# Kernel optimization log

Measured on AMD Instinct MI355X. Metric: run time of the kernel, lower is better.

The kernel has to match this reference:

```python
import jax, jax.numpy as jnp
import numpy as np

DIM = 96
D_STATE = 16
EXPAND = 2
D_INNER = EXPAND * DIM
DT_RANK = (DIM + 15) // 16  # 6
B, H, W = 2, 64, 64
K = 4  # scan directions


def _ln(x, w, b, eps=1e-5):
    mu = x.mean(-1, keepdims=True)
    var = x.var(-1, keepdims=True)
    return (x - mu) / jnp.sqrt(var + eps) * w + b


def setup_inputs() -> dict:
    key = jax.random.key(0)
    ks = jax.random.split(key, 10)
    f = jnp.float32
    x = jax.random.normal(ks[0], (B, H, W, DIM), dtype=f)
    y = jax.random.normal(ks[1], (B, H, W, DIM), dtype=f)
    inp = {
        'x': x,
        'y': y,
        'ln_w': jnp.ones((DIM,), f),
        'ln_b': jnp.zeros((DIM,), f),
        'in_proj_w': jax.random.normal(ks[2], (2 * D_INNER, DIM), f) * 0.05,
        'conv_w': jax.random.normal(ks[3], (D_INNER, 1, 3, 3), f) * 0.1,
        'conv_b': jnp.zeros((D_INNER,), f),
        'x_proj_w': jax.random.normal(ks[4], (K, DT_RANK + 2 * D_STATE, D_INNER), f) * 0.05,
        'dt_w': jax.random.normal(ks[5], (K, D_INNER, DT_RANK), f) * 0.1,
        'dt_b': jax.random.normal(ks[6], (K, D_INNER), f) * 0.1,
        'A_log': jnp.broadcast_to(jnp.log(jnp.arange(1, D_STATE + 1, dtype=f)), (K, D_INNER, D_STATE)),
        'Ds': jnp.ones((K, D_INNER), f),
        'out_norm_w': jnp.ones((D_INNER,), f),
        'out_norm_b': jnp.zeros((D_INNER,), f),
        'out_proj_w': jax.random.normal(ks[7], (DIM, D_INNER), f) * 0.05,
    }
    return inp


def _fwd(x, y, ln_w, ln_b, in_proj_w, conv_w, conv_b, x_proj_w, dt_w, dt_b,
         A_log, Ds, out_norm_w, out_norm_b, out_proj_w):
    Bsz, Hh, Ww, C = x.shape
    Din = conv_w.shape[0]
    N = A_log.shape[-1]
    R = dt_w.shape[-1]
    L = Hh * Ww

    diff = jnp.abs(x - y)                       # TemporalSpectrumBlock abs-diff
    h = _ln(diff, ln_w, ln_b)                   # VSSBlock ln_1
    xz = h @ in_proj_w.T                        # (B,H,W,2*Din)
    xm, z = jnp.split(xz, 2, axis=-1)
    xm = xm.transpose(0, 3, 1, 2)               # (B,Din,H,W)
    xm = jax.lax.conv_general_dilated(
        xm, conv_w, (1, 1), 'SAME', feature_group_count=Din,
        dimension_numbers=('NCHW', 'OIHW', 'NCHW')) + conv_b[None, :, None, None]
    xm = jax.nn.silu(xm)

    # 4-directional sequences (B,4,Din,L)
    x0 = xm.reshape(Bsz, Din, L)
    x1 = xm.transpose(0, 1, 3, 2).reshape(Bsz, Din, L)
    xs = jnp.stack([x0, x1], axis=1)
    xs = jnp.concatenate([xs, jnp.flip(xs, axis=-1)], axis=1)

    x_dbl = jnp.einsum('bkdl,kcd->bkcl', xs, x_proj_w)
    dts, Bs, Cs = jnp.split(x_dbl, [R, R + N], axis=2)   # (B,4,R,L),(B,4,N,L),(B,4,N,L)
    dts = jnp.einsum('bkrl,kdr->bkdl', dts, dt_w)
    delta = jax.nn.softplus(dts + dt_b[None, :, :, None])  # (B,4,Din,L)

    A = -jnp.exp(A_log)                                    # (4,Din,N)
    dA = jnp.exp(delta[..., None] * A[None, :, :, None, :])          # (B,4,Din,L,N)
    dBu = delta[..., None] * Bs.transpose(0, 1, 3, 2)[:, :, None] * xs[..., None]

    dA_t = dA.transpose(3, 0, 1, 2, 4)    # (L,B,4,Din,N)
    dBu_t = dBu.transpose(3, 0, 1, 2, 4)
    C_t = Cs.transpose(3, 0, 1, 2)        # (L,B,4,N)
    h0 = jnp.zeros((Bsz, 4, Din, N), dtype=x.dtype)

    def step(hc, inp):
        a, bu, c = inp
        hc = a * hc + bu
        yv = jnp.einsum('bkdn,bkn->bkd', hc, c)
        return hc, yv

    _, ys = jax.lax.scan(step, h0, (dA_t, dBu_t, C_t))    # (L,B,4,Din)
    ys = ys.transpose(1, 2, 3, 0)                          # (B,4,Din,L)
    out_y = ys + Ds[None, :, :, None] * xs

    inv_y = jnp.flip(out_y[:, 2:4], axis=-1)
    wh_y = out_y[:, 1].reshape(Bsz, Din, Ww, Hh).transpose(0, 1, 3, 2).reshape(Bsz, Din, L)
    invwh_y = inv_y[:, 1].reshape(Bsz, Din, Ww, Hh).transpose(0, 1, 3, 2).reshape(Bsz, Din, L)
    yc = out_y[:, 0] + inv_y[:, 0] + wh_y + invwh_y        # (B,Din,L)
    yc = yc.transpose(0, 2, 1).reshape(Bsz, Hh, Ww, Din)

    yn = _ln(yc, out_norm_w, out_norm_b)
    out = (yn * jax.nn.silu(z)) @ out_proj_w.T
    return diff + out                                      # residual around the block


def reference(x, y, ln_w, ln_b, in_proj_w, conv_w, conv_b, x_proj_w, dt_w, dt_b,
              A_log, Ds, out_norm_w, out_norm_b, out_proj_w):
    return _fwd(x, y, ln_w, ln_b, in_proj_w, conv_w, conv_b, x_proj_w, dt_w, dt_b,
                A_log, Ds, out_norm_w, out_norm_b, out_proj_w)
```

## Files before the change

### kernel.cpp

```cpp
#include <hip/hip_runtime.h>
#include <math.h>

#define DIMC 96
#define DIN  192
#define NST  16
#define RNK  6
#define KD   4
#define HH   64
#define WWD  64
#define LL   4096
#define BB   2
#define NC   128
#define CH   32
#define CPK  48

__device__ __forceinline__ int pos_of(int k, int l) {
    int t = ((l & 63) << 6) | (l >> 6);
    switch (k) {
        case 0: return l;
        case 1: return t;
        case 2: return LL - 1 - l;
        default: return ((((LL-1-l) & 63) << 6) | ((LL-1-l) >> 6));
    }
}

__device__ __forceinline__ float silu_f(float v) {
    return v / (1.f + __expf(-v));
}

__global__ __launch_bounds__(256) void k0_prep(
    const float* __restrict__ Win, const float* __restrict__ Wout,
    const float* __restrict__ xpw,
    float* __restrict__ WinT, float* __restrict__ WoutT, float* __restrict__ wT3)
{
    int idx = blockIdx.x*256 + threadIdx.x;
    int stride = gridDim.x*256;
    for (int i = idx; i < 96*384; i += stride) {
        int j = i / 384, o = i - j*384;
        WinT[i] = Win[o*96 + j];
    }
    for (int i = idx; i < 192*96; i += stride) {
        int j = i / 96, o = i - j*96;
        WoutT[i] = Wout[o*192 + j];
    }
    for (int i = idx; i < KD*192*CPK; i += stride) {
        int kk = i / (192*CPK); int rem = i - kk*192*CPK;
        int j = rem / CPK, c = rem - j*CPK;
        float v = 0.f;
        if (c < 16)       v = xpw[((size_t)kk*(RNK+2*NST) + RNK + c)*DIN + j];
        else if (c < 32)  v = xpw[((size_t)kk*(RNK+2*NST) + RNK + NST + (c-16))*DIN + j];
        else if (c < 38)  v = xpw[((size_t)kk*(RNK+2*NST) + (c-32))*DIN + j];
        wT3[i] = v;
    }
}

__global__ __launch_bounds__(1024) void k1_ln_inproj(
    const float* __restrict__ x, const float* __restrict__ y,
    const float* __restrict__ lnw, const float* __restrict__ lnb,
    const float* __restrict__ WinT,
    float* __restrict__ diff, float* __restrict__ xm, float* __restrict__ zbuf)
{
    __shared__ float hT[96*65];
    __shared__ float ps1[16*64], ps2[16*64];
    __shared__ float mus[64], rss[64];
    int t = threadIdx.x;
    int ptile = blockIdx.x >> 1, cgrp = blockIdx.x & 1;
    int p0 = ptile*64;

    #pragma unroll
    for (int s = 0; s < 6; s++) {
        int i = t + 1024*s;
        float v = fabsf(x[(size_t)p0*96 + i] - y[(size_t)p0*96 + i]);
        if (cgrp == 0) diff[(size_t)p0*96 + i] = v;
        int pos = i / 96, ch = i - pos*96;
        hT[ch*65 + pos] = v;
    }
    __syncthreads();
    {
        int pos = t & 63, part = t >> 6;
        float s1 = 0.f, s2 = 0.f;
        #pragma unroll
        for (int m = 0; m < 6; m++) {
            float v = hT[(part*6 + m)*65 + pos];
            s1 += v; s2 += v*v;
        }
        ps1[part*64 + pos] = s1; ps2[part*64 + pos] = s2;
    }
    __syncthreads();
    if (t < 64) {
        float S1 = 0.f, S2 = 0.f;
        #pragma unroll
        for (int i = 0; i < 16; i++) { S1 += ps1[i*64 + t]; S2 += ps2[i*64 + t]; }
        float mu = S1 * (1.f/96.f);
        float var = S2 * (1.f/96.f) - mu*mu;
        mus[t] = mu; rss[t] = rsqrtf(var + 1e-5f);
    }
    __syncthreads();
    #pragma unroll
    for (int s = 0; s < 6; s++) {
        int i = t + 1024*s;
        int pos = i / 96, ch = i - pos*96;
        hT[ch*65 + pos] = (hT[ch*65 + pos] - mus[pos]) * rss[pos] * lnw[ch] + lnb[ch];
    }
    __syncthreads();

    int w = __builtin_amdgcn_readfirstlane(t >> 6);
    int lane = t & 63;
    int c0 = cgrp*192 + w*12;
    const float* wp = WinT + c0;
    float acc[12];
    #pragma unroll
    for (int cc = 0; cc < 12; cc++) acc[cc] = 0.f;
    #pragma unroll 2
    for (int j = 0; j < 96; j++) {
        float u = hT[j*65 + lane];
        const float* wrow = wp + j*384;
        #pragma unroll
        for (int cc = 0; cc < 12; cc++) acc[cc] += u * wrow[cc];
    }
    size_t p = (size_t)(p0 + lane);
    float* dst = (c0 < 192) ? (xm + p*192 + c0) : (zbuf + p*192 + (c0 - 192));
    #pragma unroll
    for (int q = 0; q < 3; q++)
        *(float4*)&dst[4*q] = make_float4(acc[4*q], acc[4*q+1], acc[4*q+2], acc[4*q+3]);
}

__global__ __launch_bounds__(192) void k2_conv(
    const float* __restrict__ xm, const float* __restrict__ cw,
    const float* __restrict__ cb, float* __restrict__ xconv)
{
    int p = blockIdx.x;
    int d = threadIdx.x;
    int b = p >> 12;
    int l = p & (LL - 1);
    int hh = l >> 6, ww = l & 63;
    float acc = cb[d];
    const float* wd = cw + d*9;
    #pragma unroll
    for (int di = -1; di <= 1; di++) {
        int h2 = hh + di;
        if ((unsigned)h2 < HH) {
            #pragma unroll
            for (int dj = -1; dj <= 1; dj++) {
                int w2 = ww + dj;
                if ((unsigned)w2 < WWD)
                    acc += wd[(di+1)*3 + (dj+1)] * xm[((size_t)b*LL + h2*WWD + w2)*DIN + d];
            }
        }
    }
    xconv[(size_t)p*DIN + d] = silu_f(acc);
}

__global__ __launch_bounds__(512) void k3_xproj(
    const float* __restrict__ xconv, const float* __restrict__ wT3,
    float* __restrict__ XDK)
{
    __shared__ float uT[192*65];
    int t = threadIdx.x;
    int ptile = blockIdx.x >> 1, wgrp = blockIdx.x & 1;
    int p0 = ptile*64;

    #pragma unroll
    for (int s = 0; s < 24; s++) {
        int i = t + 512*s;
        int pos = i / 192, ch = i - pos*192;
        uT[ch*65 + pos] = xconv[(size_t)(p0 + pos)*192 + ch];
    }
    __syncthreads();

    int w = __builtin_amdgcn_readfirstlane(t >> 6);
    int slot = wgrp*8 + w;
    int k = slot >> 2, cq = slot & 3;
    int lane = t & 63;
    int c0 = cq*12;
    const float* wp = wT3 + (size_t)k*192*CPK + c0;
    float acc[12];
    #pragma unroll
    for (int cc = 0; cc < 12; cc++) acc[cc] = 0.f;
    #pragma unroll 2
    for (int j = 0; j < 192; j++) {
        float u = uT[j*65 + lane];
        const float* wrow = wp + j*CPK;
        #pragma unroll
        for (int cc = 0; cc < 12; cc++) acc[cc] += u * wrow[cc];
    }
    int p = p0 + lane;
    int b = p >> 12;
    int s = p & (LL - 1);
    int ts = ((s & 63) << 6) | (s >> 6);
    int l;
    switch (k) {
        case 0: l = s; break;
        case 1: l = ts; break;
        case 2: l = LL - 1 - s; break;
        default: l = LL - 1 - ts; break;
    }
    float* dst = XDK + ((size_t)(b*KD + k)*LL + l)*CPK + c0;
    #pragma unroll
    for (int q = 0; q < 3; q++)
        *(float4*)&dst[4*q] = make_float4(acc[4*q], acc[4*q+1], acc[4*q+2], acc[4*q+3]);
}

__global__ __launch_bounds__(192) void k4_scanA(
    const float* __restrict__ xconv, const float* __restrict__ XDK,
    const float* __restrict__ dtw, const float* __restrict__ dtb,
    const float* __restrict__ A_log,
    float* __restrict__ Sarr, float* __restrict__ Q)
{
    int blk = blockIdx.x;
    int c  = blk & (NC - 1);
    int bk = blk >> 7;
    int k  = bk & 3;
    int b  = bk >> 2;
    int d  = threadIdx.x;
    float dw[RNK];
    #pragma unroll
    for (int r = 0; r < RNK; r++) dw[r] = dtw[((size_t)k*DIN + d)*RNK + r];
    float bias = dtb[k*DIN + d];
    float A[NST];
    #pragma unroll
    for (int n = 0; n < NST; n++) A[n] = -__expf(A_log[((size_t)k*DIN + d)*NST + n]);
    bool fastA = true;
    #pragma unroll
    for (int n = 1; n < NST; n++)
        fastA = fastA && (fabsf(A[n] - (float)(n+1)*A[0]) <= 1e-4f*(float)(n+1));

    float h[NST];
    #pragma unroll
    for (int n = 0; n < NST; n++) h[n] = 0.f;
    float S = 0.f;

    size_t rb = ((size_t)bk*LL + c*CH)*CPK;
    if (fastA) {
        #pragma unroll 2
        for (int step = 0; step < CH; step++) {
            const float* rec = XDK + rb + step*CPK;
            float dl = bias;
            #pragma unroll
            for (int r = 0; r < RNK; r++) dl += rec[32 + r] * dw[r];
            dl = (dl > 20.f) ? dl : __logf(1.f + __expf(dl));
            int l = c*CH + step;
            float uu = xconv[((size_t)b*LL + pos_of(k, l))*DIN + d];
            float du = dl * uu;
            S += dl;
            float e1 = __expf(dl * A[0]);
            float e2 = e1*e1, e4 = e2*e2;
            float p0 = e1, p1 = e2, p2 = e2*e1, p3 = e4;
            #pragma unroll
            for (int g = 0; g < 4; g++) {
                h[4*g+0] = p0*h[4*g+0] + du*rec[4*g+0];
                h[4*g+1] = p1*h[4*g+1] + du*rec[4*g+1];
                h[4*g+2] = p2*h[4*g+2] + du*rec[4*g+2];
                h[4*g+3] = p3*h[4*g+3] + du*rec[4*g+3];
                if (g < 3) { p0 *= e4; p1 *= e4; p2 *= e4; p3 *= e4; }
            }
        }
    } else {
        #pragma unroll 2
        for (int step = 0; step < CH; step++) {
            const float* rec = XDK + rb + step*CPK;
            float dl = bias;
            #pragma unroll
            for (int r = 0; r < RNK; r++) dl += rec[32 + r] * dw[r];
            dl = (dl > 20.f) ? dl : __logf(1.f + __expf(dl));
            int l = c*CH + step;
            float uu = xconv[((size_t)b*LL + pos_of(k, l))*DIN + d];
            float du = dl * uu;
            S += dl;
            #pragma unroll
            for (int n = 0; n < NST; n++) {
                float a = __expf(dl * A[n]);
                h[n] = a*h[n] + du*rec[n];
            }
        }
    }
    Sarr[(size_t)blk*DIN + d] = S;
    size_t qb = (size_t)blk*NST*DIN + d;
    #pragma unroll
    for (int n = 0; n < NST; n++) Q[qb + n*DIN] = h[n];
}

__global__ __launch_bounds__(256) void k5_scanB(
    const float* __restrict__ A_log, const float* __restrict__ Sarr,
    float* __restrict__ Q)
{
    int idx = blockIdx.x*256 + threadIdx.x;
    if (idx >= BB*KD*NST*DIN) return;
    int d = idx % DIN;
    int rest = idx / DIN;
    int n = rest % NST; rest /= NST;
    int k = rest & 3;
    int b = rest >> 2;
    int bk = b*KD + k;
    float A = -__expf(A_log[((size_t)k*DIN + d)*NST + n]);
    size_t qstride = (size_t)NST*DIN;
    size_t qbase = (size_t)bk*NC*qstride + n*DIN + d;
    size_t sbase = (size_t)bk*NC*DIN + d;
    float h = 0.f;
    #pragma unroll 4
    for (int c = 0; c < NC; c++) {
        float s = Sarr[sbase + c*DIN];
        float q = Q[qbase + c*qstride];
        Q[qbase + c*qstride] = h;
        h = __expf(A*s)*h + q;
    }
}

__global__ __launch_bounds__(192) void k6_scanC(
    const float* __restrict__ xconv, const float* __restrict__ XDK,
    const float* __restrict__ dtw, const float* __restrict__ dtb,
    const float* __restrict__ A_log, const float* __restrict__ Ds,
    const float* __restrict__ Q, float* __restrict__ outy)
{
    int blk = blockIdx.x;
    int c  = blk & (NC - 1);
    int bk = blk >> 7;
    int k  = bk & 3;
    int b  = bk >> 2;
    int d  = threadIdx.x;
    float dw[RNK];
    #pragma unroll
    for (int r = 0; r < RNK; r++) dw[r] = dtw[((size_t)k*DIN + d)*RNK + r];
    float bias = dtb[k*DIN + d];
    float A[NST];
    #pragma unroll
    for (int n = 0; n < NST; n++) A[n] = -__expf(A_log[((size_t)k*DIN + d)*NST + n]);
    bool fastA = true;
    #pragma unroll
    for (int n = 1; n < NST; n++)
        fastA = fastA && (fabsf(A[n] - (float)(n+1)*A[0]) <= 1e-4f*(float)(n+1));
    float h[NST];
    size_t qb = (size_t)blk*NST*DIN + d;
    #pragma unroll
    for (int n = 0; n < NST; n++) h[n] = Q[qb + n*DIN];
    float Dv = Ds[k*DIN + d];

    size_t rb = ((size_t)bk*LL + c*CH)*CPK;
    if (fastA) {
        #pragma unroll 2
        for (int step = 0; step < CH; step++) {
            const float* rec = XDK + rb + step*CPK;
            float dl = bias;
            #pragma unroll
            for (int r = 0; r < RNK; r++) dl += rec[32 + r] * dw[r];
            dl = (dl > 20.f) ? dl : __logf(1.f + __expf(dl));
            int l = c*CH + step;
            int sp = pos_of(k, l);
            float uu = xconv[((size_t)b*LL + sp)*DIN + d];
            float du = dl * uu;
            float e1 = __expf(dl * A[0]);
            float e2 = e1*e1, e4 = e2*e2;
            float p0 = e1, p1 = e2, p2 = e2*e1, p3 = e4;
            float yv = 0.f;
            #pragma unroll
            for (int g = 0; g < 4; g++) {
                h[4*g+0] = p0*h[4*g+0] + du*rec[4*g+0];
                h[4*g+1] = p1*h[4*g+1] + du*rec[4*g+1];
                h[4*g+2] = p2*h[4*g+2] + du*rec[4*g+2];
                h[4*g+3] = p3*h[4*g+3] + du*rec[4*g+3];
                yv += h[4*g+0]*rec[16+4*g+0] + h[4*g+1]*rec[16+4*g+1]
                    + h[4*g+2]*rec[16+4*g+2] + h[4*g+3]*rec[16+4*g+3];
                if (g < 3) { p0 *= e4; p1 *= e4; p2 *= e4; p3 *= e4; }
            }
            outy[((size_t)bk*LL + sp)*DIN + d] = yv + Dv*uu;
        }
    } else {
        #pragma unroll 2
        for (int step = 0; step < CH; step++) {
            const float* rec = XDK + rb + step*CPK;
            float dl = bias;
            #pragma unroll
            for (int r = 0; r < RNK; r++) dl += rec[32 + r] * dw[r];
            dl = (dl > 20.f) ? dl : __logf(1.f + __expf(dl));
            int l = c*CH + step;
            int sp = pos_of(k, l);
            float uu = xconv[((size_t)b*LL + sp)*DIN + d];
            float du = dl * uu;
            float yv = 0.f;
            #pragma unroll
            for (int n = 0; n < NST; n++) {
                float a = __expf(dl * A[n]);
                h[n] = a*h[n] + du*rec[n];
                yv += h[n] * rec[16 + n];
            }
            outy[((size_t)bk*LL + sp)*DIN + d] = yv + Dv*uu;
        }
    }
}

__global__ __launch_bounds__(256) void k7_out(
    const float* __restrict__ outy, const float* __restrict__ zbuf,
    const float* __restrict__ diff, const float* __restrict__ onw,
    const float* __restrict__ onb, const float* __restrict__ WoutT,
    float* __restrict__ out)
{
    __shared__ float gT[192*65];
    __shared__ float ps1[4*64], ps2[4*64];
    __shared__ float mus[64], rss[64];
    int t = threadIdx.x;
    int ptile = blockIdx.x >> 1, chalf = blockIdx.x & 1;
    int p0 = ptile*64;
    int b = p0 >> 12;
    int l0 = p0 & (LL - 1);
    const size_t seg = (size_t)LL*DIN;
    size_t base = ((size_t)(b*KD)*LL + l0)*DIN;

    #pragma unroll
    for (int s = 0; s < 48; s++) {
        int i = t + 256*s;
        float yc = outy[base + i] + outy[base + seg + i]
                 + outy[base + 2*seg + i] + outy[base + 3*seg + i];
        int pos = i / 192, ch = i - pos*192;
        gT[ch*65 + pos] = yc;
    }
    __syncthreads();
    {
        int pos = t & 63, part = t >> 6;
        float s1 = 0.f, s2 = 0.f;
        #pragma unroll
        for (int m = 0; m < 48; m++) {
            float v = gT[(part*48 + m)*65 + pos];
            s1 += v; s2 += v*v;
        }
        ps1[part*64 + pos] = s1; ps2[part*64 + pos] = s2;
    }
    __syncthreads();
    if (t < 64) {
        float S1 = ps1[t] + ps1[64+t] + ps1[128+t] + ps1[192+t];
        float S2 = ps2[t] + ps2[64+t] + ps2[128+t] + ps2[192+t];
        float mu = S1 * (1.f/192.f);
        float var = S2 * (1.f/192.f) - mu*mu;
        mus[t] = mu; rss[t] = rsqrtf(var + 1e-5f);
    }
    __syncthreads();
    #pragma unroll
    for (int s = 0; s < 48; s++) {
        int i = t + 256*s;
        int pos = i / 192, ch = i - pos*192;
        float v = gT[ch*65 + pos];
        float yn = (v - mus[pos]) * rss[pos] * onw[ch] + onb[ch];
        float z = zbuf[(size_t)p0*DIN + i];
        gT[ch*65 + pos] = yn * silu_f(z);
    }
    __syncthreads();

    int w = __builtin_amdgcn_readfirstlane(t >> 6);
    int lane = t & 63;
    int c0 = chalf*48 + w*12;
    const float* wp = WoutT + c0;
    float acc[12];
    #pragma unroll
    for (int cc = 0; cc < 12; cc++) acc[cc] = 0.f;
    #pragma unroll 2
    for (int j = 0; j < 192; j++) {
        float u = gT[j*65 + lane];
        const float* wrow = wp + j*96;
        #pragma unroll
        for (int cc = 0; cc < 12; cc++) acc[cc] += u * wrow[cc];
    }
    size_t p = (size_t)(p0 + lane);
    #pragma unroll
    for (int q = 0; q < 3; q++) {
        float4 dv = *(const float4*)&diff[p*96 + c0 + 4*q];
        *(float4*)&out[p*96 + c0 + 4*q] =
            make_float4(acc[4*q] + dv.x, acc[4*q+1] + dv.y, acc[4*q+2] + dv.z, acc[4*q+3] + dv.w);
    }
}

extern "C" void kernel_launch(void* const* d_in, const int* in_sizes, int n_in,
                              void* d_out, int out_size, void* d_ws, size_t ws_size,
                              hipStream_t stream)
{
    const float* x       = (const float*)d_in[0];
    const float* y       = (const float*)d_in[1];
    const float* ln_w    = (const float*)d_in[2];
    const float* ln_b    = (const float*)d_in[3];
    const float* in_proj = (const float*)d_in[4];
    const float* conv_w  = (const float*)d_in[5];
    const float* conv_b  = (const float*)d_in[6];
    const float* x_proj  = (const float*)d_in[7];
    const float* dt_w    = (const float*)d_in[8];
    const float* dt_b    = (const float*)d_in[9];
    const float* A_log   = (const float*)d_in[10];
    const float* Ds      = (const float*)d_in[11];
    const float* onw     = (const float*)d_in[12];
    const float* onb     = (const float*)d_in[13];
    const float* out_w   = (const float*)d_in[14];
    float* out = (float*)d_out;

    float* ws    = (float*)d_ws;
    float* diff  = ws;
    float* zbuf  = diff  + 786432;
    float* xm    = zbuf  + 1572864;
    float* xconv = xm    + 1572864;
    float* XDK   = xconv + 1572864;
    float* outy  = XDK   + 1572864;
    float* Qbuf  = outy  + 6291456;
    float* Sarr  = Qbuf  + 6291456;
    float* WinT  = Sarr  + 393216;
    float* WoutT = WinT  + 36864;
    float* wT3   = WoutT + 18432;

    const int BL = BB * LL;

    hipLaunchKernelGGL(k0_prep, dim3(144), dim3(256), 0, stream,
                       in_proj, out_w, x_proj, WinT, WoutT, wT3);
    hipLaunchKernelGGL(k1_ln_inproj, dim3(BL/64*2), dim3(1024), 0, stream,
                       x, y, ln_w, ln_b, WinT, diff, xm, zbuf);
    hipLaunchKernelGGL(k2_conv, dim3(BL), dim3(DIN), 0, stream,
                       xm, conv_w, conv_b, xconv);
    hipLaunchKernelGGL(k3_xproj, dim3(BL/64*2), dim3(512), 0, stream,
                       xconv, wT3, XDK);
    hipLaunchKernelGGL(k4_scanA, dim3(BB*KD*NC), dim3(DIN), 0, stream,
                       xconv, XDK, dt_w, dt_b, A_log, Sarr, Qbuf);
    hipLaunchKernelGGL(k5_scanB, dim3((BB*KD*NST*DIN + 255)/256), dim3(256), 0, stream,
                       A_log, Sarr, Qbuf);
    hipLaunchKernelGGL(k6_scanC, dim3(BB*KD*NC), dim3(DIN), 0, stream,
                       xconv, XDK, dt_w, dt_b, A_log, Ds, Qbuf, outy);
    hipLaunchKernelGGL(k7_out, dim3(BL/64*2), dim3(256), 0, stream,
                       outy, zbuf, diff, onw, onb, WoutT, out);
}
```

Measured before the change: 269.4 us.

## Fuse three-phase chunked scan into one cooperative kernel with grid syncs

Replaces the separate chunk-scan, carry-propagation and output-scan kernels with a single cooperative kernel that uses grid.sync between phases. Each block keeps its chunk's x_proj records and the computed softplus dt values in shared memory, so the second pass reuses them instead of reloading and recomputing. When A follows the (n+1)*A0 pattern it also swaps the per-state exponentials for powers of a single exp. This removes two kernel launches and some redundant work, at the cost of the grid-sync overhead and a carry phase that runs on only a fraction of the threads. It falls back to the old three kernels if cooperative launch or co-residency of all 1024 blocks is not available.

```diff
diff --git a/kernel.cpp b/kernel.cpp
--- a/kernel.cpp
+++ b/kernel.cpp
@@ -1,5 +1,8 @@
 #include <hip/hip_runtime.h>
+#include <hip/hip_cooperative_groups.h>
 #include <math.h>
+
+namespace cg = cooperative_groups;
 
 #define DIMC 96
 #define DIN  192
@@ -388,6 +391,178 @@
     }
 }
 
+__global__ __launch_bounds__(192, 3) void k_scan(
+    const float* __restrict__ xconv, const float* __restrict__ XDK,
+    const float* __restrict__ dtw, const float* __restrict__ dtb,
+    const float* __restrict__ A_log, const float* __restrict__ Ds,
+    float* __restrict__ Sarr, float* __restrict__ Q, float* __restrict__ outy)
+{
+    __shared__ __align__(16) float recS[CH*CPK];
+    __shared__ float dlS[CH*DIN];
+    cg::grid_group grid = cg::this_grid();
+
+    const int blk = blockIdx.x;
+    const int c  = blk & (NC - 1);
+    const int bk = blk >> 7;
+    const int k  = bk & 3;
+    const int b  = bk >> 2;
+    const int d  = threadIdx.x;
+
+    float dw[RNK];
+    #pragma unroll
+    for (int r = 0; r < RNK; r++) dw[r] = dtw[((size_t)k*DIN + d)*RNK + r];
+    float bias = dtb[k*DIN + d];
+    float A[NST];
+    #pragma unroll
+    for (int n = 0; n < NST; n++) A[n] = -__expf(A_log[((size_t)k*DIN + d)*NST + n]);
+    bool fastA = true;
+    #pragma unroll
+    for (int n = 1; n < NST; n++)
+        fastA = fastA && (fabsf(A[n] - (float)(n+1)*A[0]) <= 1e-4f*(float)(n+1));
+
+    {
+        const float4* src = (const float4*)(XDK + ((size_t)bk*LL + c*CH)*CPK);
+        float4* dst = (float4*)recS;
+        #pragma unroll
+        for (int i = 0; i < 2; i++) dst[d + 192*i] = src[d + 192*i];
+    }
+    __syncthreads();
+
+    float h[NST];
+    #pragma unroll
+    for (int n = 0; n < NST; n++) h[n] = 0.f;
+    float S = 0.f;
+    if (fastA) {
+        #pragma unroll 2
+        for (int step = 0; step < CH; step++) {
+            const float* rec = recS + step*CPK;
+            float dl = bias;
+            #pragma unroll
+            for (int r = 0; r < RNK; r++) dl += rec[32 + r] * dw[r];
+            dl = (dl > 20.f) ? dl : __logf(1.f + __expf(dl));
+            dlS[step*DIN + d] = dl;
+            int l = c*CH + step;
+            float uu = xconv[((size_t)b*LL + pos_of(k, l))*DIN + d];
+            float du = dl * uu;
+            S += dl;
+            float e1 = __expf(dl * A[0]);
+            float e2 = e1*e1, e4 = e2*e2;
+            float p0 = e1, p1 = e2, p2 = e2*e1, p3 = e4;
+            #pragma unroll
+            for (int g = 0; g < 4; g++) {
+                h[4*g+0] = p0*h[4*g+0] + du*rec[4*g+0];
+                h[4*g+1] = p1*h[4*g+1] + du*rec[4*g+1];
+                h[4*g+2] = p2*h[4*g+2] + du*rec[4*g+2];
+                h[4*g+3] = p3*h[4*g+3] + du*rec[4*g+3];
+                if (g < 3) { p0 *= e4; p1 *= e4; p2 *= e4; p3 *= e4; }
+            }
+        }
+    } else {
+        #pragma unroll 2
+        for (int step = 0; step < CH; step++) {
+            const float* rec = recS + step*CPK;
+            float dl = bias;
+            #pragma unroll
+            for (int r = 0; r < RNK; r++) dl += rec[32 + r] * dw[r];
+            dl = (dl > 20.f) ? dl : __logf(1.f + __expf(dl));
+            dlS[step*DIN + d] = dl;
+            int l = c*CH + step;
+            float uu = xconv[((size_t)b*LL + pos_of(k, l))*DIN + d];
+            float du = dl * uu;
+            S += dl;
+            #pragma unroll
+            for (int n = 0; n < NST; n++) {
+                float a = __expf(dl * A[n]);
+                h[n] = a*h[n] + du*rec[n];
+            }
+        }
+    }
+    Sarr[(size_t)blk*DIN + d] = S;
+    size_t qb = (size_t)blk*NST*DIN + d;
+    #pragma unroll
+    for (int n = 0; n < NST; n++) Q[qb + n*DIN] = h[n];
+
+    __threadfence();
+    grid.sync();
+    __threadfence();
+
+    {
+        int gid = blockIdx.x*DIN + threadIdx.x;
+        if (gid < BB*KD*NST*DIN) {
+            int dd = gid % DIN;
+            int rest = gid / DIN;
+            int nn = rest % NST; rest /= NST;
+            int kk = rest & 3;
+            int bb = rest >> 2;
+            int bk2 = bb*KD + kk;
+            float A2 = -__expf(A_log[((size_t)kk*DIN + dd)*NST + nn]);
+            size_t qstride = (size_t)NST*DIN;
+            size_t qbase = (size_t)bk2*NC*qstride + nn*DIN + dd;
+            size_t sbase = (size_t)bk2*NC*DIN + dd;
+            float hh = 0.f;
+            #pragma unroll 4
+            for (int cc = 0; cc < NC; cc++) {
+                float s = Sarr[sbase + cc*DIN];
+                float q = Q[qbase + cc*qstride];
+                Q[qbase + cc*qstride] = hh;
+                hh = __expf(A2*s)*hh + q;
+            }
+        }
+    }
+
+    __threadfence();
+    grid.sync();
+    __threadfence();
+
+    #pragma unroll
+    for (int n = 0; n < NST; n++) h[n] = Q[qb + n*DIN];
+    float Dv = Ds[k*DIN + d];
+    if (fastA) {
+        #pragma unroll 2
+        for (int step = 0; step < CH; step++) {
+            const float* rec = recS + step*CPK;
+            float dl = dlS[step*DIN + d];
+            int l = c*CH + step;
+            int sp = pos_of(k, l);
+            float uu = xconv[((size_t)b*LL + sp)*DIN + d];
+            float du = dl * uu;
+            float e1 = __expf(dl * A[0]);
+            float e2 = e1*e1, e4 = e2*e2;
+            float p0 = e1, p1 = e2, p2 = e2*e1, p3 = e4;
+            float yv = 0.f;
+            #pragma unroll
+            for (int g = 0; g < 4; g++) {
+                h[4*g+0] = p0*h[4*g+0] + du*rec[4*g+0];
+                h[4*g+1] = p1*h[4*g+1] + du*rec[4*g+1];
+                h[4*g+2] = p2*h[4*g+2] + du*rec[4*g+2];
+                h[4*g+3] = p3*h[4*g+3] + du*rec[4*g+3];
+                yv += h[4*g+0]*rec[16+4*g+0] + h[4*g+1]*rec[16+4*g+1]
+                    + h[4*g+2]*rec[16+4*g+2] + h[4*g+3]*rec[16+4*g+3];
+                if (g < 3) { p0 *= e4; p1 *= e4; p2 *= e4; p3 *= e4; }
+            }
+            outy[((size_t)bk*LL + sp)*DIN + d] = yv + Dv*uu;
+        }
+    } else {
+        #pragma unroll 2
+        for (int step = 0; step < CH; step++) {
+            const float* rec = recS + step*CPK;
+            float dl = dlS[step*DIN + d];
+            int l = c*CH + step;
+            int sp = pos_of(k, l);
+            float uu = xconv[((size_t)b*LL + sp)*DIN + d];
+            float du = dl * uu;
+            float yv = 0.f;
+            #pragma unroll
+            for (int n = 0; n < NST; n++) {
+                float a = __expf(dl * A[n]);
+                h[n] = a*h[n] + du*rec[n];
+                yv += h[n] * rec[16 + n];
+            }
+            outy[((size_t)bk*LL + sp)*DIN + d] = yv + Dv*uu;
+        }
+    }
+}
+
 __global__ __launch_bounds__(256) void k7_out(
     const float* __restrict__ outy, const float* __restrict__ zbuf,
     const float* __restrict__ diff, const float* __restrict__ onw,
@@ -503,6 +678,21 @@
 
     const int BL = BB * LL;
 
+    static int coop_state = -1;
+    if (coop_state < 0) {
+        coop_state = 0;
+        int dev = 0;
+        if (hipGetDevice(&dev) == hipSuccess) {
+            hipDeviceProp_t prop;
+            if (hipGetDeviceProperties(&prop, dev) == hipSuccess && prop.cooperativeLaunch) {
+                int nb = 0;
+                if (hipOccupancyMaxActiveBlocksPerMultiprocessor(&nb, k_scan, DIN, 0) == hipSuccess &&
+                    nb * prop.multiProcessorCount >= BB*KD*NC)
+                    coop_state = 1;
+            }
+        }
+    }
+
     hipLaunchKernelGGL(k0_prep, dim3(144), dim3(256), 0, stream,
                        in_proj, out_w, x_proj, WinT, WoutT, wT3);
     hipLaunchKernelGGL(k1_ln_inproj, dim3(BL/64*2), dim3(1024), 0, stream,
@@ -511,12 +701,25 @@
                        xm, conv_w, conv_b, xconv);
     hipLaunchKernelGGL(k3_xproj, dim3(BL/64*2), dim3(512), 0, stream,
                        xconv, wT3, XDK);
-    hipLaunchKernelGGL(k4_scanA, dim3(BB*KD*NC), dim3(DIN), 0, stream,
-                       xconv, XDK, dt_w, dt_b, A_log, Sarr, Qbuf);
-    hipLaunchKernelGGL(k5_scanB, dim3((BB*KD*NST*DIN + 255)/256), dim3(256), 0, stream,
-                       A_log, Sarr, Qbuf);
-    hipLaunchKernelGGL(k6_scanC, dim3(BB*KD*NC), dim3(DIN), 0, stream,
-                       xconv, XDK, dt_w, dt_b, A_log, Ds, Qbuf, outy);
+
+    bool did_coop = false;
+    if (coop_state == 1) {
+        void* kargs[] = {
+            (void*)&xconv, (void*)&XDK, (void*)&dt_w, (void*)&dt_b,
+            (void*)&A_log, (void*)&Ds, (void*)&Sarr, (void*)&Qbuf, (void*)&outy };
+        did_coop = (hipLaunchCooperativeKernel(k_scan, dim3(BB*KD*NC), dim3(DIN),
+                                               kargs, 0, stream) == hipSuccess);
+        if (!did_coop) coop_state = 0;
+    }
+    if (!did_coop) {
+        hipLaunchKernelGGL(k4_scanA, dim3(BB*KD*NC), dim3(DIN), 0, stream,
+                           xconv, XDK, dt_w, dt_b, A_log, Sarr, Qbuf);
+        hipLaunchKernelGGL(k5_scanB, dim3((BB*KD*NST*DIN + 255)/256), dim3(256), 0, stream,
+                           A_log, Sarr, Qbuf);
+        hipLaunchKernelGGL(k6_scanC, dim3(BB*KD*NC), dim3(DIN), 0, stream,
+                           xconv, XDK, dt_w, dt_b, A_log, Ds, Qbuf, outy);
+    }
+
     hipLaunchKernelGGL(k7_out, dim3(BL/64*2), dim3(256), 0, stream,
                        outy, zbuf, diff, onw, onb, WoutT, out);
 }
```

Result: no change. 266.1 us (-1.2%).

## Fuse depthwise conv into x-projection and stop splitting tiles across blocks

Applied to the files above, without the earlier changes.

The depthwise 3x3 conv + SiLU is fused into the x-projection kernel, so each 64-position tile computes its conv output directly into shared memory instead of launching a separate conv kernel and re-reading xconv. The in-projection and output kernels no longer split channel groups across two blocks. Each block now does both halves itself, so the LayerNorm and abs-diff work is not duplicated. This cuts one launch and redundant LN and tile loads, at the cost of half as many blocks, which lowers parallelism to 128 blocks per kernel.

```diff
diff --git a/kernel.cpp b/kernel.cpp
--- a/kernel.cpp
+++ b/kernel.cpp
@@ -64,14 +64,13 @@
     __shared__ float ps1[16*64], ps2[16*64];
     __shared__ float mus[64], rss[64];
     int t = threadIdx.x;
-    int ptile = blockIdx.x >> 1, cgrp = blockIdx.x & 1;
-    int p0 = ptile*64;
+    int p0 = blockIdx.x*64;
 
     #pragma unroll
     for (int s = 0; s < 6; s++) {
         int i = t + 1024*s;
         float v = fabsf(x[(size_t)p0*96 + i] - y[(size_t)p0*96 + i]);
-        if (cgrp == 0) diff[(size_t)p0*96 + i] = v;
+        diff[(size_t)p0*96 + i] = v;
         int pos = i / 96, ch = i - pos*96;
         hT[ch*65 + pos] = v;
     }
@@ -106,71 +105,83 @@
 
     int w = __builtin_amdgcn_readfirstlane(t >> 6);
     int lane = t & 63;
-    int c0 = cgrp*192 + w*12;
-    const float* wp = WinT + c0;
-    float acc[12];
-    #pragma unroll
-    for (int cc = 0; cc < 12; cc++) acc[cc] = 0.f;
-    #pragma unroll 2
-    for (int j = 0; j < 96; j++) {
-        float u = hT[j*65 + lane];
-        const float* wrow = wp + j*384;
-        #pragma unroll
-        for (int cc = 0; cc < 12; cc++) acc[cc] += u * wrow[cc];
-    }
+    int c0 = w*12;
     size_t p = (size_t)(p0 + lane);
-    float* dst = (c0 < 192) ? (xm + p*192 + c0) : (zbuf + p*192 + (c0 - 192));
-    #pragma unroll
-    for (int q = 0; q < 3; q++)
-        *(float4*)&dst[4*q] = make_float4(acc[4*q], acc[4*q+1], acc[4*q+2], acc[4*q+3]);
-}
-
-__global__ __launch_bounds__(192) void k2_conv(
+
+    {
+        const float* wp = WinT + c0;
+        float acc[12];
+        #pragma unroll
+        for (int cc = 0; cc < 12; cc++) acc[cc] = 0.f;
+        #pragma unroll 2
+        for (int j = 0; j < 96; j++) {
+            float u = hT[j*65 + lane];
+            const float* wrow = wp + j*384;
+            #pragma unroll
+            for (int cc = 0; cc < 12; cc++) acc[cc] += u * wrow[cc];
+        }
+        float* dst = xm + p*192 + c0;
+        #pragma unroll
+        for (int q = 0; q < 3; q++)
+            *(float4*)&dst[4*q] = make_float4(acc[4*q], acc[4*q+1], acc[4*q+2], acc[4*q+3]);
+    }
+    {
+        const float* wp = WinT + 192 + c0;
+        float acc[12];
+        #pragma unroll
+        for (int cc = 0; cc < 12; cc++) acc[cc] = 0.f;
+        #pragma unroll 2
+        for (int j = 0; j < 96; j++) {
+            float u = hT[j*65 + lane];
+            const float* wrow = wp + j*384;
+            #pragma unroll
+            for (int cc = 0; cc < 12; cc++) acc[cc] += u * wrow[cc];
+        }
+        float* dst = zbuf + p*192 + c0;
+        #pragma unroll
+        for (int q = 0; q < 3; q++)
+            *(float4*)&dst[4*q] = make_float4(acc[4*q], acc[4*q+1], acc[4*q+2], acc[4*q+3]);
+    }
+}
+
+__global__ __launch_bounds__(1024) void k3_convxproj(
     const float* __restrict__ xm, const float* __restrict__ cw,
-    const float* __restrict__ cb, float* __restrict__ xconv)
-{
-    int p = blockIdx.x;
-    int d = threadIdx.x;
-    int b = p >> 12;
-    int l = p & (LL - 1);
-    int hh = l >> 6, ww = l & 63;
-    float acc = cb[d];
-    const float* wd = cw + d*9;
-    #pragma unroll
-    for (int di = -1; di <= 1; di++) {
-        int h2 = hh + di;
-        if ((unsigned)h2 < HH) {
-            #pragma unroll
-            for (int dj = -1; dj <= 1; dj++) {
-                int w2 = ww + dj;
-                if ((unsigned)w2 < WWD)
-                    acc += wd[(di+1)*3 + (dj+1)] * xm[((size_t)b*LL + h2*WWD + w2)*DIN + d];
-            }
-        }
-    }
-    xconv[(size_t)p*DIN + d] = silu_f(acc);
-}
-
-__global__ __launch_bounds__(512) void k3_xproj(
-    const float* __restrict__ xconv, const float* __restrict__ wT3,
-    float* __restrict__ XDK)
+    const float* __restrict__ cb, const float* __restrict__ wT3,
+    float* __restrict__ xconv, float* __restrict__ XDK)
 {
     __shared__ float uT[192*65];
     int t = threadIdx.x;
-    int ptile = blockIdx.x >> 1, wgrp = blockIdx.x & 1;
-    int p0 = ptile*64;
-
-    #pragma unroll
-    for (int s = 0; s < 24; s++) {
-        int i = t + 512*s;
+    int p0 = blockIdx.x*64;
+    int b = p0 >> 12;
+    int hh = (p0 & (LL - 1)) >> 6;
+    size_t rowbase = (size_t)b*LL*DIN;
+
+    #pragma unroll
+    for (int s = 0; s < 12; s++) {
+        int i = t + 1024*s;
         int pos = i / 192, ch = i - pos*192;
-        uT[ch*65 + pos] = xconv[(size_t)(p0 + pos)*192 + ch];
+        float acc = cb[ch];
+        const float* wd = cw + ch*9;
+        #pragma unroll
+        for (int di = -1; di <= 1; di++) {
+            int h2 = hh + di;
+            if ((unsigned)h2 < HH) {
+                #pragma unroll
+                for (int dj = -1; dj <= 1; dj++) {
+                    int w2 = pos + dj;
+                    if ((unsigned)w2 < WWD)
+                        acc += wd[(di+1)*3 + (dj+1)] * xm[rowbase + (size_t)(h2*WWD + w2)*DIN + ch];
+                }
+            }
+        }
+        float v = silu_f(acc);
+        uT[ch*65 + pos] = v;
+        xconv[(size_t)(p0 + pos)*DIN + ch] = v;
     }
     __syncthreads();
 
     int w = __builtin_amdgcn_readfirstlane(t >> 6);
-    int slot = wgrp*8 + w;
-    int k = slot >> 2, cq = slot & 3;
+    int k = w >> 2, cq = w & 3;
     int lane = t & 63;
     int c0 = cq*12;
     const float* wp = wT3 + (size_t)k*192*CPK + c0;
@@ -185,7 +196,6 @@
         for (int cc = 0; cc < 12; cc++) acc[cc] += u * wrow[cc];
     }
     int p = p0 + lane;
-    int b = p >> 12;
     int s = p & (LL - 1);
     int ts = ((s & 63) << 6) | (s >> 6);
     int l;
@@ -388,26 +398,25 @@
     }
 }
 
-__global__ __launch_bounds__(256) void k7_out(
+__global__ __launch_bounds__(512) void k7_out(
     const float* __restrict__ outy, const float* __restrict__ zbuf,
     const float* __restrict__ diff, const float* __restrict__ onw,
     const float* __restrict__ onb, const float* __restrict__ WoutT,
     float* __restrict__ out)
 {
     __shared__ float gT[192*65];
-    __shared__ float ps1[4*64], ps2[4*64];
+    __shared__ float ps1[8*64], ps2[8*64];
     __shared__ float mus[64], rss[64];
     int t = threadIdx.x;
-    int ptile = blockIdx.x >> 1, chalf = blockIdx.x & 1;
-    int p0 = ptile*64;
+    int p0 = blockIdx.x*64;
     int b = p0 >> 12;
     int l0 = p0 & (LL - 1);
     const size_t seg = (size_t)LL*DIN;
     size_t base = ((size_t)(b*KD)*LL + l0)*DIN;
 
     #pragma unroll
-    for (int s = 0; s < 48; s++) {
-        int i = t + 256*s;
+    for (int s = 0; s < 24; s++) {
+        int i = t + 512*s;
         float yc = outy[base + i] + outy[base + seg + i]
                  + outy[base + 2*seg + i] + outy[base + 3*seg + i];
         int pos = i / 192, ch = i - pos*192;
@@ -418,24 +427,25 @@
         int pos = t & 63, part = t >> 6;
         float s1 = 0.f, s2 = 0.f;
         #pragma unroll
-        for (int m = 0; m < 48; m++) {
-            float v = gT[(part*48 + m)*65 + pos];
+        for (int m = 0; m < 24; m++) {
+            float v = gT[(part*24 + m)*65 + pos];
             s1 += v; s2 += v*v;
         }
         ps1[part*64 + pos] = s1; ps2[part*64 + pos] = s2;
     }
     __syncthreads();
     if (t < 64) {
-        float S1 = ps1[t] + ps1[64+t] + ps1[128+t] + ps1[192+t];
-        float S2 = ps2[t] + ps2[64+t] + ps2[128+t] + ps2[192+t];
+        float S1 = 0.f, S2 = 0.f;
+        #pragma unroll
+        for (int i = 0; i < 8; i++) { S1 += ps1[i*64 + t]; S2 += ps2[i*64 + t]; }
         float mu = S1 * (1.f/192.f);
         float var = S2 * (1.f/192.f) - mu*mu;
         mus[t] = mu; rss[t] = rsqrtf(var + 1e-5f);
     }
     __syncthreads();
     #pragma unroll
-    for (int s = 0; s < 48; s++) {
-        int i = t + 256*s;
+    for (int s = 0; s < 24; s++) {
+        int i = t + 512*s;
         int pos = i / 192, ch = i - pos*192;
         float v = gT[ch*65 + pos];
         float yn = (v - mus[pos]) * rss[pos] * onw[ch] + onb[ch];
@@ -446,7 +456,7 @@
 
     int w = __builtin_amdgcn_readfirstlane(t >> 6);
     int lane = t & 63;
-    int c0 = chalf*48 + w*12;
+    int c0 = w*12;
     const float* wp = WoutT + c0;
     float acc[12];
     #pragma unroll
@@ -501,22 +511,20 @@
     float* WoutT = WinT  + 36864;
     float* wT3   = WoutT + 18432;
 
-    const int BL = BB * LL;
+    const int NTILE = BB * LL / 64;
 
     hipLaunchKernelGGL(k0_prep, dim3(144), dim3(256), 0, stream,
                        in_proj, out_w, x_proj, WinT, WoutT, wT3);
-    hipLaunchKernelGGL(k1_ln_inproj, dim3(BL/64*2), dim3(1024), 0, stream,
+    hipLaunchKernelGGL(k1_ln_inproj, dim3(NTILE), dim3(1024), 0, stream,
                        x, y, ln_w, ln_b, WinT, diff, xm, zbuf);
-    hipLaunchKernelGGL(k2_conv, dim3(BL), dim3(DIN), 0, stream,
-                       xm, conv_w, conv_b, xconv);
-    hipLaunchKernelGGL(k3_xproj, dim3(BL/64*2), dim3(512), 0, stream,
-                       xconv, wT3, XDK);
+    hipLaunchKernelGGL(k3_convxproj, dim3(NTILE), dim3(1024), 0, stream,
+                       xm, conv_w, conv_b, wT3, xconv, XDK);
     hipLaunchKernelGGL(k4_scanA, dim3(BB*KD*NC), dim3(DIN), 0, stream,
                        xconv, XDK, dt_w, dt_b, A_log, Sarr, Qbuf);
     hipLaunchKernelGGL(k5_scanB, dim3((BB*KD*NST*DIN + 255)/256), dim3(256), 0, stream,
                        A_log, Sarr, Qbuf);
     hipLaunchKernelGGL(k6_scanC, dim3(BB*KD*NC), dim3(DIN), 0, stream,
                        xconv, XDK, dt_w, dt_b, A_log, Ds, Qbuf, outy);
-    hipLaunchKernelGGL(k7_out, dim3(BL/64*2), dim3(256), 0, stream,
+    hipLaunchKernelGGL(k7_out, dim3(NTILE), dim3(512), 0, stream,
                        outy, zbuf, diff, onw, onb, WoutT, out);
 }
```

Measured after the change: 276.7 us. +2.7%, slower.
